# Optimization experiments

Measured on AMD Instinct MI355X. Metric: run time of the kernel, lower is better.

Reference implementation:

```python
import jax, jax.numpy as jnp
import numpy as np

INPUTDIM = 256
OUTDIM = 64
GRIDSIZE = 300
BATCH = 2048


def setup_inputs() -> dict:
    key = jax.random.key(0)
    kx, kw = jax.random.split(key)
    x = jax.random.normal(kx, (BATCH, INPUTDIM), dtype=jnp.float32)
    stddev = 1.0 / (np.sqrt(INPUTDIM) * np.sqrt(GRIDSIZE))
    fouriercoeffs = jax.random.normal(kw, (2, OUTDIM, INPUTDIM, GRIDSIZE), dtype=jnp.float32) * stddev
    return {"x": x, "fouriercoeffs": fouriercoeffs}


def reference(x, fouriercoeffs):
    # k: frequencies 1..gridsize, shape [gridsize]
    gridsize = fouriercoeffs.shape[-1]
    k = jnp.arange(1, gridsize + 1, dtype=x.dtype)
    # phase [batch, inputdim, gridsize]
    phase = x[:, :, None] * k[None, None, :]
    c = jnp.cos(phase)
    s = jnp.sin(phase)
    # y[b,j] = sum_{i,k} c[b,i,k]*Wc[j,i,k] + s[b,i,k]*Ws[j,i,k]
    y = jnp.einsum('bik,jik->bj', c, fouriercoeffs[0]) + jnp.einsum('bik,jik->bj', s, fouriercoeffs[1])
    return y
```

## Files before the change

### kernel.cpp

```cpp
#include <hip/hip_runtime.h>
#include <hip/hip_bf16.h>

#define BATCH 2048
#define IDIM  256
#define ODIM  64
#define GRIDN 300

typedef __bf16 bf16x8 __attribute__((ext_vector_type(8)));
typedef float  f32x16 __attribute__((ext_vector_type(16)));
typedef float  f32x2  __attribute__((ext_vector_type(2)));
typedef unsigned int uint4v __attribute__((ext_vector_type(4)));

__device__ __forceinline__ unsigned short f2bf(float f) {
    return __builtin_bit_cast(unsigned short, __float2bfloat16(f));
}

__global__ __launch_bounds__(256) void fkan_prep(const float* __restrict__ fc,
                                                 char* __restrict__ wp) {
    __shared__ alignas(16) char lds[32768];
    const int blk = blockIdx.x;
    const int ib  = blk & 15;
    const int gb  = blk >> 4;
    const int g0  = gb * 8;
    const int G   = (gb == 37) ? 4 : 8;
    const int q   = threadIdx.x >> 6;
    const int j   = threadIdx.x & 63;

    float vals[2][4][8];
    #pragma unroll
    for (int t = 0; t < 2; ++t) {
        #pragma unroll
        for (int e = 0; e < 4; ++e) {
            const float* src = fc + (((size_t)t * ODIM + j) * IDIM
                                     + (ib * 16 + q * 4 + e)) * GRIDN + g0;
            float4 lo = *(const float4*)(src);
            vals[t][e][0] = lo.x; vals[t][e][1] = lo.y;
            vals[t][e][2] = lo.z; vals[t][e][3] = lo.w;
            if (G == 8) {
                float4 hi = *(const float4*)(src + 4);
                vals[t][e][4] = hi.x; vals[t][e][5] = hi.y;
                vals[t][e][6] = hi.z; vals[t][e][7] = hi.w;
            }
        }
    }
    #pragma unroll
    for (int g = 0; g < 8; ++g) {
        if (g < 4 || G == 8) {
            uint4v dw;
            #pragma unroll
            for (int e = 0; e < 4; ++e)
                dw[e] = (unsigned)f2bf(vals[0][e][g]) | ((unsigned)f2bf(vals[1][e][g]) << 16);
            *(uint4v*)(lds + g * 4096 + q * 1024 + j * 16) = dw;
        }
    }
    __syncthreads();
    char* dst = wp + ((size_t)ib * GRIDN + g0) * 4096;
    for (int w = threadIdx.x * 16; w < G * 4096; w += 256 * 16)
        *(uint4v*)(dst + w) = *(const uint4v*)(lds + w);
}

__global__ __launch_bounds__(256, 4) void fkan_main(const float* __restrict__ x,
                                                    const char* __restrict__ wp,
                                                    float* __restrict__ out) {
    const int bid    = blockIdx.x;
    const int xcd    = bid & 7;
    const int within = bid >> 3;
    const int slice  = xcd * 8 + (within & 7);
    const int mtile  = within >> 3;
    const int isplit = slice >> 2;
    const int gq     = slice & 3;
    const int g_begin = gq * 75;

    const int tid  = threadIdx.x;
    const int wave = tid >> 6;
    const int lane = tid & 63;
    const int l31  = lane & 31;
    const int kgrp = lane >> 5;
    const int row  = mtile * 128 + wave * 32 + l31;

    f32x2 vc[4], vs[4], vbc[4], vbs[4], vnbs[4];
    const float* xrow = x + (size_t)row * IDIM + isplit * 16;
    #pragma unroll
    for (int h = 0; h < 2; ++h) {
        const float4 xv4 = *(const float4*)(xrow + h * 8 + kgrp * 4);
        float xa[4] = {xv4.x, xv4.y, xv4.z, xv4.w};
        #pragma unroll
        for (int p = 0; p < 4; ++p) {
            const int ss = h * 4 + p;
            const float xv = xa[p];
            float sb, cb;
            __sincosf(xv, &sb, &cb);
            vbc[ss >> 1][ss & 1] = cb; vbs[ss >> 1][ss & 1] = sb;
            vnbs[ss >> 1][ss & 1] = -sb;
            float s0 = sb, c0 = cb;
            if (g_begin != 0) __sincosf((float)(g_begin + 1) * xv, &s0, &c0);
            vc[ss >> 1][ss & 1] = c0; vs[ss >> 1][ss & 1] = s0;
        }
    }

    const unsigned aq = (unsigned)kgrp * 1024 + (unsigned)l31 * 16;
    const char* curp = wp + ((size_t)(isplit * GRIDN + g_begin)) * 4096 + aq;

    bf16x8 c0 = *(const bf16x8*)(curp);
    bf16x8 c1 = *(const bf16x8*)(curp + 512);
    bf16x8 c2 = *(const bf16x8*)(curp + 2048);
    bf16x8 c3 = *(const bf16x8*)(curp + 2560);

    f32x16 acc0 = {0,0,0,0,0,0,0,0,0,0,0,0,0,0,0,0};
    f32x16 acc1 = {0,0,0,0,0,0,0,0,0,0,0,0,0,0,0,0};

    #pragma unroll 2
    for (int it = 0; it < 75; ++it) {
        const char* np = curp + (it < 74 ? 4096 : 0);
        const bf16x8 n0 = *(const bf16x8*)(np);
        const bf16x8 n1 = *(const bf16x8*)(np + 512);
        const bf16x8 n2 = *(const bf16x8*)(np + 2048);
        const bf16x8 n3 = *(const bf16x8*)(np + 2560);

        uint4v a1, a2;
        #pragma unroll
        for (int p = 0; p < 4; ++p) {
            const float c1f = vc[p >> 1][p & 1],       s1f = vs[p >> 1][p & 1];
            const float c2f = vc[2 + (p >> 1)][p & 1], s2f = vs[2 + (p >> 1)][p & 1];
            unsigned r1, r2;
            asm("v_cvt_pk_bf16_f32 %0, %1, %2" : "=v"(r1) : "v"(c1f), "v"(s1f));
            asm("v_cvt_pk_bf16_f32 %0, %1, %2" : "=v"(r2) : "v"(c2f), "v"(s2f));
            a1[p] = r1; a2[p] = r2;
        }
        const bf16x8 af1 = __builtin_bit_cast(bf16x8, a1);
        const bf16x8 af2 = __builtin_bit_cast(bf16x8, a2);
        __builtin_amdgcn_s_setprio(1);
        acc0 = __builtin_amdgcn_mfma_f32_32x32x16_bf16(af1, c0, acc0, 0, 0, 0);
        acc1 = __builtin_amdgcn_mfma_f32_32x32x16_bf16(af1, c1, acc1, 0, 0, 0);
        acc0 = __builtin_amdgcn_mfma_f32_32x32x16_bf16(af2, c2, acc0, 0, 0, 0);
        acc1 = __builtin_amdgcn_mfma_f32_32x32x16_bf16(af2, c3, acc1, 0, 0, 0);
        __builtin_amdgcn_s_setprio(0);
        #pragma unroll
        for (int qq = 0; qq < 4; ++qq) {
            f32x2 t, u, cn, sn;
            asm("v_pk_mul_f32 %0, %1, %2" : "=v"(t) : "v"(vs[qq]), "v"(vnbs[qq]));
            asm("v_pk_mul_f32 %0, %1, %2" : "=v"(u) : "v"(vc[qq]), "v"(vbs[qq]));
            asm("v_pk_fma_f32 %0, %1, %2, %3" : "=v"(cn) : "v"(vc[qq]), "v"(vbc[qq]), "v"(t));
            asm("v_pk_fma_f32 %0, %1, %2, %3" : "=v"(sn) : "v"(vs[qq]), "v"(vbc[qq]), "v"(u));
            vc[qq] = cn; vs[qq] = sn;
        }
        c0 = n0; c1 = n1; c2 = n2; c3 = n3;
        curp = np;
    }

    #pragma unroll
    for (int r = 0; r < 16; ++r) {
        const int orow = mtile * 128 + wave * 32 + (r & 3) + 8 * (r >> 2) + 4 * kgrp;
        unsafeAtomicAdd(out + (size_t)orow * ODIM + l31, acc0[r]);
        unsafeAtomicAdd(out + (size_t)orow * ODIM + 32 + l31, acc1[r]);
    }
}

__global__ __launch_bounds__(256) void fkan_naive(const float* __restrict__ x,
                                                  const float* __restrict__ fc,
                                                  float* __restrict__ out) {
    const int j = blockIdx.x >> 3;
    const int b = (blockIdx.x & 7) * 256 + threadIdx.x;
    const float* xr = x + (size_t)b * IDIM;
    float acc = 0.f;
    for (int i = 0; i < IDIM; ++i) {
        const float xv = xr[i];
        float sb, cb;
        __sincosf(xv, &sb, &cb);
        float c = cb, s = sb;
        const float* wc = fc + ((size_t)j * IDIM + i) * GRIDN;
        const float* ws = wc + (size_t)ODIM * IDIM * GRIDN;
        for (int g = 0; g < GRIDN; ++g) {
            acc += c * wc[g] + s * ws[g];
            const float cn = c * cb - s * sb;
            s = s * cb + c * sb;
            c = cn;
        }
    }
    out[(size_t)b * ODIM + j] = acc;
}

extern "C" void kernel_launch(void* const* d_in, const int* in_sizes, int n_in,
                              void* d_out, int out_size, void* d_ws, size_t ws_size,
                              hipStream_t stream) {
    const float* x  = (const float*)d_in[0];
    const float* fc = (const float*)d_in[1];
    float* out = (float*)d_out;
    constexpr size_t WPB = 16ull * GRIDN * 4096;

    if (ws_size >= WPB) {
        hipMemsetAsync(d_out, 0, (size_t)out_size * sizeof(float), stream);
        fkan_prep<<<608, 256, 0, stream>>>(fc, (char*)d_ws);
        fkan_main<<<1024, 256, 0, stream>>>(x, (const char*)d_ws, out);
    } else {
        fkan_naive<<<512, 256, 0, stream>>>(x, fc, out);
    }
}
```

Measured before the change: 86.17 us.

## Replace global atomics with in-block LDS reduction plus partial-sum reduce kernel

Remaps the work so the four waves in a block cover different input slices of the same 32 batch rows. Their MFMA accumulators are summed through shared memory, and each block writes one partial tile into a workspace buffer. A separate reduce kernel sums the 16 partials per output element. This removes the memset and the many float atomics on the output, at the cost of an extra kernel launch, 8 MB of partial-buffer traffic, and a barrier plus LDS round trip in the main kernel.

```diff
diff --git a/kernel.cpp b/kernel.cpp
--- a/kernel.cpp
+++ b/kernel.cpp
@@ -8,6 +8,7 @@
 
 typedef __bf16 bf16x8 __attribute__((ext_vector_type(8)));
 typedef float  f32x16 __attribute__((ext_vector_type(16)));
+typedef float  f32x4  __attribute__((ext_vector_type(4)));
 typedef float  f32x2  __attribute__((ext_vector_type(2)));
 typedef unsigned int uint4v __attribute__((ext_vector_type(4)));
 
@@ -61,14 +62,16 @@
 
 __global__ __launch_bounds__(256, 4) void fkan_main(const float* __restrict__ x,
                                                     const char* __restrict__ wp,
-                                                    float* __restrict__ out) {
+                                                    float* __restrict__ part) {
+    __shared__ float red[4][32][64];
+
     const int bid    = blockIdx.x;
     const int xcd    = bid & 7;
     const int within = bid >> 3;
-    const int slice  = xcd * 8 + (within & 7);
-    const int mtile  = within >> 3;
-    const int isplit = slice >> 2;
-    const int gq     = slice & 3;
+    const int kg     = xcd * 2 + (within & 1);
+    const int mt     = within >> 1;
+    const int iq     = kg >> 2;
+    const int gq     = kg & 3;
     const int g_begin = gq * 75;
 
     const int tid  = threadIdx.x;
@@ -76,7 +79,8 @@
     const int lane = tid & 63;
     const int l31  = lane & 31;
     const int kgrp = lane >> 5;
-    const int row  = mtile * 128 + wave * 32 + l31;
+    const int isplit = iq * 4 + wave;
+    const int row  = mt * 32 + l31;
 
     f32x2 vc[4], vs[4], vbc[4], vbs[4], vnbs[4];
     const float* xrow = x + (size_t)row * IDIM + isplit * 16;
@@ -150,10 +154,35 @@
 
     #pragma unroll
     for (int r = 0; r < 16; ++r) {
-        const int orow = mtile * 128 + wave * 32 + (r & 3) + 8 * (r >> 2) + 4 * kgrp;
-        unsafeAtomicAdd(out + (size_t)orow * ODIM + l31, acc0[r]);
-        unsafeAtomicAdd(out + (size_t)orow * ODIM + 32 + l31, acc1[r]);
-    }
+        const int rbase = (r & 3) + 8 * (r >> 2) + 4 * kgrp;
+        red[wave][rbase][l31]      = acc0[r];
+        red[wave][rbase][32 + l31] = acc1[r];
+    }
+    __syncthreads();
+    {
+        const int row2 = wave * 8 + (lane >> 3);
+        const int col0 = (lane & 7) * 8;
+        f32x4 sA = *(const f32x4*)(&red[0][row2][col0]);
+        f32x4 sB = *(const f32x4*)(&red[0][row2][col0 + 4]);
+        #pragma unroll
+        for (int w2 = 1; w2 < 4; ++w2) {
+            sA += *(const f32x4*)(&red[w2][row2][col0]);
+            sB += *(const f32x4*)(&red[w2][row2][col0 + 4]);
+        }
+        float* dst = part + ((size_t)kg * BATCH + mt * 32 + row2) * ODIM + col0;
+        *(f32x4*)(dst)     = sA;
+        *(f32x4*)(dst + 4) = sB;
+    }
+}
+
+__global__ __launch_bounds__(256) void fkan_reduce(const float* __restrict__ part,
+                                                   float* __restrict__ out) {
+    const int idx = blockIdx.x * 256 + threadIdx.x;
+    float s = 0.f;
+    #pragma unroll
+    for (int k = 0; k < 16; ++k)
+        s += part[(size_t)k * (BATCH * ODIM) + idx];
+    out[idx] = s;
 }
 
 __global__ __launch_bounds__(256) void fkan_naive(const float* __restrict__ x,
@@ -186,12 +215,15 @@
     const float* x  = (const float*)d_in[0];
     const float* fc = (const float*)d_in[1];
     float* out = (float*)d_out;
-    constexpr size_t WPB = 16ull * GRIDN * 4096;
-
-    if (ws_size >= WPB) {
-        hipMemsetAsync(d_out, 0, (size_t)out_size * sizeof(float), stream);
-        fkan_prep<<<608, 256, 0, stream>>>(fc, (char*)d_ws);
-        fkan_main<<<1024, 256, 0, stream>>>(x, (const char*)d_ws, out);
+    constexpr size_t WPB  = 16ull * GRIDN * 4096;
+    constexpr size_t PART = 16ull * BATCH * ODIM * 4;
+
+    if (ws_size >= WPB + PART) {
+        char*  wp   = (char*)d_ws;
+        float* part = (float*)((char*)d_ws + WPB);
+        fkan_prep<<<608, 256, 0, stream>>>(fc, wp);
+        fkan_main<<<1024, 256, 0, stream>>>(x, wp, part);
+        fkan_reduce<<<512, 256, 0, stream>>>(part, out);
     } else {
         fkan_naive<<<512, 256, 0, stream>>>(x, fc, out);
     }
```

Measured after the change: 77.46 us. -10.1%, faster.
